# Performance work log

Measured on AMD Instinct MI355X. Metric: run time of the kernel, lower is better.

## Reference

```python
import jax, jax.numpy as jnp
import numpy as np

N_NODES = 20000   # max_childs
N_EDGES = 640000
FEAT = 256        # node_feat_size
HID = 128         # node_hidden_size
NUM_SEM = 57
EDGE_TYPES = 4
EDGE_FEAT = 8


def setup_inputs() -> dict:
    key = jax.random.key(0)
    ks = jax.random.split(key, 10)
    inp = {
        "child_feats": jax.random.normal(ks[0], (1, N_NODES, FEAT + NUM_SEM), jnp.float32),
        "child_exists": jnp.ones((1, N_NODES, 1), jnp.float32),
        "edge_type_onehot": jax.random.uniform(ks[1], (1, N_EDGES, EDGE_TYPES), jnp.float32),
        "edge_feats": jax.random.normal(ks[2], (1, N_EDGES, EDGE_FEAT), jnp.float32),
        "edge_indices": jax.random.randint(ks[3], (1, N_EDGES, 2), 0, N_NODES, jnp.int64 if jax.config.jax_enable_x64 else jnp.int32),
        "W_child": jax.random.normal(ks[4], (FEAT + NUM_SEM, HID), jnp.float32) * 0.05,
        "b_child": jnp.zeros((HID,), jnp.float32),
        "W_edge0": jax.random.normal(ks[5], (2 * HID + EDGE_FEAT + EDGE_TYPES, HID), jnp.float32) * 0.05,
        "b_edge0": jnp.zeros((HID,), jnp.float32),
        "W_edge1": jax.random.normal(ks[6], (2 * HID + EDGE_FEAT + EDGE_TYPES, HID), jnp.float32) * 0.05,
        "b_edge1": jnp.zeros((HID,), jnp.float32),
        "W_parent": jax.random.normal(ks[7], (3 * HID, FEAT), jnp.float32) * 0.05,
        "b_parent": jnp.zeros((FEAT,), jnp.float32),
    }
    return inp


def reference(child_feats, child_exists, edge_type_onehot, edge_feats, edge_indices,
              W_child, b_child, W_edge0, b_edge0, W_edge1, b_edge1, W_parent, b_parent):
    # child_op + existence mask: [1, N, FEAT+NUM_SEM] -> [N, HID]
    h = jax.nn.relu(child_feats @ W_child + b_child) * child_exists
    h = h[0]  # batch_size is hard-coded to 1 in the original module

    # symmetric_type == 'max': pool over children
    iter_parent_feats = [jnp.max(h, axis=0)]

    # edge features: cat(edge_type_onehot, edge_feats) -> [E, ET+EF]
    ef = jnp.concatenate([edge_type_onehot[0], edge_feats[0]], axis=1)
    src = edge_indices[0, :, 0]
    dst = edge_indices[0, :, 1]

    for W, b in ((W_edge0, b_edge0), (W_edge1, b_edge1)):
        # gather -> per-edge MLP: [E, 2*HID + ET + EF] -> [E, HID]
        msg = jax.nn.relu(jnp.concatenate([h[src], h[dst], ef], axis=1) @ W + b)
        # edge_symmetric_type == 'max' with zero-initialized out buffer:
        # result = max(0, segment_max(msg)) per node
        h = jnp.maximum(jax.ops.segment_max(msg, src, num_segments=N_NODES), 0.0)
        iter_parent_feats.append(jnp.max(h, axis=0))

    parent = jnp.concatenate(iter_parent_feats)[None, :]  # [1, 3*HID]
    return jax.nn.relu(parent @ W_parent + b_parent)       # [1, FEAT]
```

## Files before the change

kernel.cpp:

```cpp
#include <hip/hip_runtime.h>

#define N_NODES   20000
#define N_EDGES   640000
#define CF        313
#define KC        320
#define ROWB      640

typedef __attribute__((ext_vector_type(8))) short short8;
typedef __attribute__((ext_vector_type(4))) float f32x4;
typedef __attribute__((ext_vector_type(4))) unsigned short u16x4;
typedef float f32x4u __attribute__((ext_vector_type(4), aligned(4)));
typedef _Float16 h2 __attribute__((ext_vector_type(2)));

static __device__ __forceinline__ unsigned short f2bf(float f) {
    unsigned u = __float_as_uint(f);
    u = u + 0x7FFFu + ((u >> 16) & 1u);
    return (unsigned short)(u >> 16);
}
static __device__ __forceinline__ int pkh(float a, float b) {
    h2 h; h.x = (_Float16)a; h.y = (_Float16)b;
    return __builtin_bit_cast(int, h);
}
static __device__ __forceinline__ h2 bch(int v) { return __builtin_bit_cast(h2, v); }
static __device__ __forceinline__ float dot2f(h2 a, h2 b, float c) {
    return __builtin_amdgcn_fdot2(a, b, c, false);
}

__global__ void setup_kernel(const float* __restrict__ Wc,
                             const float* __restrict__ We0,
                             const float* __restrict__ We1,
                             const int* __restrict__ eidx,
                             unsigned short* __restrict__ WcT,
                             unsigned short* __restrict__ Wab0,
                             unsigned short* __restrict__ Wab1,
                             unsigned* __restrict__ hist) {
    const int b = blockIdx.x, tid = threadIdx.x;
    if (b < 416) {
        int g = b * 256 + tid;
        if (g < 128 * KC) {
            int n = g / KC, k = g % KC;
            WcT[g] = f2bf(k < CF ? Wc[k * 128 + n] : 0.f);
        } else if (g < 128 * KC + 32768) {
            int h = g - 128 * KC;
            int n = h >> 7, k = h & 127;
            Wab0[h] = f2bf(n < 128 ? We0[k * 128 + n] : We0[(128 + k) * 128 + (n - 128)]);
        } else {
            int h = g - 128 * KC - 32768;
            int n = h >> 7, k = h & 127;
            Wab1[h] = f2bf(n < 128 ? We1[k * 128 + n] : We1[(128 + k) * 128 + (n - 128)]);
        }
    } else {
        int e = (b - 416) * 256 + tid;
        if (e < N_EDGES) atomicAdd(hist + eidx[2 * e], 1u);
    }
}

__global__ void scan_kernel(const unsigned* __restrict__ hist,
                            unsigned* __restrict__ cursor,
                            unsigned* __restrict__ cstart,
                            unsigned* __restrict__ parent) {
    __shared__ unsigned part[1024];
    int t = threadIdx.x;
    if (t < 384) parent[t] = 0;
    unsigned loc[20];
    unsigned s = 0;
    int base = t * 20;
    if (t < 1000) {
        #pragma unroll
        for (int i = 0; i < 20; ++i) { loc[i] = hist[base + i]; s += loc[i]; }
    }
    part[t] = s;
    __syncthreads();
    for (int off = 1; off < 1024; off <<= 1) {
        unsigned u = (t >= off) ? part[t - off] : 0u;
        __syncthreads();
        part[t] += u;
        __syncthreads();
    }
    if (t < 1000) {
        unsigned run = part[t] - s;
        #pragma unroll
        for (int i = 0; i < 20; ++i) {
            cursor[base + i] = run;
            cstart[base + i] = run;
            run += loc[i];
        }
    }
}

__global__ void scatter_kernel(const int* __restrict__ eidx,
                               const float* __restrict__ onehot,
                               const float* __restrict__ efeat,
                               unsigned* __restrict__ cursor,
                               int4* __restrict__ es) {
    int e = blockIdx.x * 256 + threadIdx.x;
    if (e >= N_EDGES) return;
    int2 sd = ((const int2*)eidx)[e];
    unsigned pos = atomicAdd(cursor + sd.x, 1u);
    float4 oh = *(const float4*)(onehot + 4 * (size_t)e);
    float4 ea = *(const float4*)(efeat + 8 * (size_t)e);
    float4 eb = *(const float4*)(efeat + 8 * (size_t)e + 4);
    int4 w0, w1;
    w0.x = sd.y;
    w0.y = pkh(oh.x, oh.y); w0.z = pkh(oh.z, oh.w); w0.w = pkh(ea.x, ea.y);
    w1.x = pkh(ea.z, ea.w); w1.y = pkh(eb.x, eb.y); w1.z = pkh(eb.z, eb.w);
    w1.w = 0;
    es[2 * (size_t)pos]     = w0;
    es[2 * (size_t)pos + 1] = w1;
}

__global__ __launch_bounds__(256)
void child_ab(const float* __restrict__ cf,
              const float* __restrict__ exists,
              const unsigned short* __restrict__ WcT,
              const float* __restrict__ bc,
              const unsigned short* __restrict__ Wab,
              const float* __restrict__ be,
              float* __restrict__ Afl,
              unsigned short* __restrict__ Bbf,
              unsigned int* __restrict__ pmax) {
    __shared__ __align__(16) unsigned char Alds[64 * ROWB];
    __shared__ __align__(16) unsigned char Hlds[64 * 256];

    const int tid  = threadIdx.x;
    const int lane = tid & 63;
    const int wave = tid >> 6;
    const int row0 = blockIdx.x * 64;

    const int n0c = wave * 32;
    short8 bfrag[10][2];
    {
        int col  = n0c + (lane & 15);
        int krow = (lane >> 4) * 8;
        #pragma unroll
        for (int ks = 0; ks < 10; ++ks)
            #pragma unroll
            for (int nt = 0; nt < 2; ++nt)
                bfrag[ks][nt] = *(const short8*)(WcT + (col + nt * 16) * KC + ks * 32 + krow);
    }
    float bvc[2];
    bvc[0] = bc[n0c + (lane & 15)];
    bvc[1] = bc[n0c + 16 + (lane & 15)];

    {
        int r = tid >> 2, p = tid & 3;
        int node = row0 + r;
        bool valid = node < N_NODES;
        const float* g = cf + (size_t)node * CF;
        unsigned rbase = r * ROWB;
        unsigned sw = (r & 7) << 4;
        #pragma unroll
        for (int i = 0; i < 10; ++i) {
            int c = p + i * 4;
            short8 v = {};
            if (valid) {
                if (c < 39) {
                    f32x4u a0 = *(const f32x4u*)(g + c * 8);
                    f32x4u a1 = *(const f32x4u*)(g + c * 8 + 4);
                    v[0] = (short)f2bf(a0.x); v[1] = (short)f2bf(a0.y);
                    v[2] = (short)f2bf(a0.z); v[3] = (short)f2bf(a0.w);
                    v[4] = (short)f2bf(a1.x); v[5] = (short)f2bf(a1.y);
                    v[6] = (short)f2bf(a1.z); v[7] = (short)f2bf(a1.w);
                } else {
                    v[0] = (short)f2bf(g[312]);
                }
            }
            *(short8*)(Alds + ((rbase + c * 16) ^ sw)) = v;
        }
    }
    __syncthreads();

    f32x4 acc[4][2] = {};
    {
        int arow = lane & 15;
        unsigned kb = (lane >> 4) * 16;
        #pragma unroll
        for (int ks = 0; ks < 10; ++ks)
            #pragma unroll
            for (int mt = 0; mt < 4; ++mt) {
                int row = mt * 16 + arow;
                short8 a = *(const short8*)(Alds + (((unsigned)row * ROWB + ks * 64 + kb) ^ ((row & 7) << 4)));
                acc[mt][0] = __builtin_amdgcn_mfma_f32_16x16x32_bf16(a, bfrag[ks][0], acc[mt][0], 0, 0, 0);
                acc[mt][1] = __builtin_amdgcn_mfma_f32_16x16x32_bf16(a, bfrag[ks][1], acc[mt][1], 0, 0, 0);
            }
    }

    {
        int rb = (lane >> 4) * 4;
        #pragma unroll
        for (int nt = 0; nt < 2; ++nt) {
            int col = n0c + nt * 16 + (lane & 15);
            float m = 0.f;
            #pragma unroll
            for (int mt = 0; mt < 4; ++mt)
                #pragma unroll
                for (int j = 0; j < 4; ++j) {
                    int r = mt * 16 + rb + j;
                    int node = row0 + r;
                    float v = 0.f;
                    if (node < N_NODES)
                        v = fmaxf(acc[mt][nt][j] + bvc[nt], 0.f) * exists[node];
                    *(unsigned short*)(Hlds + (((unsigned)r * 256 + col * 2) ^ ((r & 7) << 4))) = f2bf(v);
                    m = fmaxf(m, v);
                }
            m = fmaxf(m, __shfl_xor(m, 16));
            m = fmaxf(m, __shfl_xor(m, 32));
            if ((lane >> 4) == 0)
                atomicMax(pmax + col, __float_as_uint(m));
        }
    }
    __syncthreads();

    const int n0 = wave * 64;
    const int krow = (lane >> 4) * 8;
    short8 bfrag2[4][4];
    {
        int colb = n0 + (lane & 15);
        #pragma unroll
        for (int ks = 0; ks < 4; ++ks)
            #pragma unroll
            for (int nt = 0; nt < 4; ++nt)
                bfrag2[ks][nt] = *(const short8*)(Wab + (colb + nt * 16) * 128 + ks * 32 + krow);
    }

    f32x4 acc2[4][4] = {};
    #pragma unroll
    for (int ks = 0; ks < 4; ++ks)
        #pragma unroll
        for (int mt = 0; mt < 4; ++mt) {
            int r = mt * 16 + (lane & 15);
            short8 a = *(const short8*)(Hlds + (((unsigned)r * 256 + ks * 64 + krow * 2) ^ ((r & 7) << 4)));
            #pragma unroll
            for (int nt = 0; nt < 4; ++nt)
                acc2[mt][nt] = __builtin_amdgcn_mfma_f32_16x16x32_bf16(a, bfrag2[ks][nt], acc2[mt][nt], 0, 0, 0);
        }

    {
        int rb = (lane >> 4) * 4;
        #pragma unroll
        for (int nt = 0; nt < 4; ++nt) {
            int col = n0 + nt * 16 + (lane & 15);
            float badd = (col < 128) ? be[col] : 0.f;
            #pragma unroll
            for (int mt = 0; mt < 4; ++mt)
                #pragma unroll
                for (int j = 0; j < 4; ++j) {
                    int row = row0 + mt * 16 + rb + j;
                    if (row < N_NODES) {
                        float v = acc2[mt][nt][j] + badd;
                        if (col < 128) Afl[(size_t)row * 128 + col] = v;
                        else           Bbf[(size_t)row * 128 + col - 128] = f2bf(v);
                    }
                }
        }
    }
}

__global__ __launch_bounds__(256)
void gemmAB(const unsigned short* __restrict__ hbf,
            const unsigned short* __restrict__ WT,
            const float* __restrict__ bias,
            float* __restrict__ Afl,
            unsigned short* __restrict__ Bbf) {
    const int tid  = threadIdx.x;
    const int lane = tid & 63;
    const int wave = tid >> 6;
    const int n0   = wave * 64;
    const int row0 = blockIdx.x * 32;
    const int krow = (lane >> 4) * 8;

    short8 bfrag[4][4];
    {
        int colb = n0 + (lane & 15);
        #pragma unroll
        for (int ks = 0; ks < 4; ++ks)
            #pragma unroll
            for (int nt = 0; nt < 4; ++nt)
                bfrag[ks][nt] = *(const short8*)(WT + (colb + nt * 16) * 128 + ks * 32 + krow);
    }

    f32x4 acc[2][4] = {};
    #pragma unroll
    for (int ks = 0; ks < 4; ++ks)
        #pragma unroll
        for (int mt = 0; mt < 2; ++mt) {
            int row = row0 + mt * 16 + (lane & 15);
            short8 a = *(const short8*)(hbf + (size_t)row * 128 + ks * 32 + krow);
            #pragma unroll
            for (int nt = 0; nt < 4; ++nt)
                acc[mt][nt] = __builtin_amdgcn_mfma_f32_16x16x32_bf16(a, bfrag[ks][nt], acc[mt][nt], 0, 0, 0);
        }

    {
        int rb = (lane >> 4) * 4;
        #pragma unroll
        for (int nt = 0; nt < 4; ++nt) {
            int col = n0 + nt * 16 + (lane & 15);
            float badd = (col < 128) ? bias[col] : 0.f;
            #pragma unroll
            for (int mt = 0; mt < 2; ++mt)
                #pragma unroll
                for (int j = 0; j < 4; ++j) {
                    int row = row0 + mt * 16 + rb + j;
                    float v = acc[mt][nt][j] + badd;
                    if (col < 128) Afl[(size_t)row * 128 + col] = v;
                    else           Bbf[(size_t)row * 128 + col - 128] = f2bf(v);
                }
        }
    }
}

__global__ __launch_bounds__(256, 3)
void edge_pass(const unsigned short* __restrict__ Bbf,
               const float* __restrict__ Afl,
               const int4* __restrict__ es,
               const float* __restrict__ Wef,
               const unsigned* __restrict__ cstart,
               const unsigned* __restrict__ hist,
               unsigned short* __restrict__ hbf,
               unsigned* __restrict__ pslice) {
    __shared__ unsigned cmax[128];
    const int tid = threadIdx.x;
    if (tid < 128) cmax[tid] = 0;
    __syncthreads();

    const int s  = blockIdx.x * 8 + (tid >> 5);
    const int c0 = (tid & 31) * 4;

    float4 a = *(const float4*)(Afl + (size_t)s * 128 + c0);

    h2 wf[6][4];
    #pragma unroll
    for (int kp = 0; kp < 6; ++kp)
        #pragma unroll
        for (int j = 0; j < 4; ++j) {
            h2 w;
            w.x = (_Float16)Wef[(2 * kp) * 128 + c0 + j];
            w.y = (_Float16)Wef[(2 * kp + 1) * 128 + c0 + j];
            wf[kp][j] = w;
        }

    float m0 = -1e30f, m1 = -1e30f, m2 = -1e30f, m3 = -1e30f;
    const unsigned cnt = hist[s];
    if (cnt) {
        const unsigned last = cnt - 1;
        const unsigned cb = cstart[s] * 32u;
        const char* esb = (const char*)es;
        const unsigned short* bbase = Bbf + c0;

        unsigned dstv[12];
        int4 ra[3], rb[3];
        u16x4 bv[6];

        #pragma unroll
        for (int k = 0; k < 12; ++k)
            dstv[k] = *(const unsigned*)(esb + cb + min((unsigned)k, last) * 32u);
        #pragma unroll
        for (int k = 0; k < 3; ++k) {
            const int4* q = (const int4*)(esb + cb + min((unsigned)k, last) * 32u);
            ra[k] = q[0]; rb[k] = q[1];
        }
        #pragma unroll
        for (int k = 0; k < 6; ++k)
            bv[k] = *(const u16x4*)(bbase + (size_t)dstv[k] * 128);

        const unsigned niter = (cnt + 11) / 12;
        for (unsigned it = 0; it < niter; ++it) {
            const unsigned jb = it * 12;
            #pragma unroll
            for (int u = 0; u < 12; ++u) {
                int4 RA = ra[u % 3], RB = rb[u % 3];
                u16x4 B = bv[u % 6];
                h2 e0 = bch(RA.y), e1 = bch(RA.z), e2 = bch(RA.w);
                h2 e3 = bch(RB.x), e4 = bch(RB.y), e5 = bch(RB.z);

                float x0 = __uint_as_float(((unsigned)(unsigned short)B[0]) << 16);
                float x1 = __uint_as_float(((unsigned)(unsigned short)B[1]) << 16);
                float x2 = __uint_as_float(((unsigned)(unsigned short)B[2]) << 16);
                float x3 = __uint_as_float(((unsigned)(unsigned short)B[3]) << 16);
                x0 = dot2f(e0, wf[0][0], x0); x1 = dot2f(e0, wf[0][1], x1);
                x2 = dot2f(e0, wf[0][2], x2); x3 = dot2f(e0, wf[0][3], x3);
                x0 = dot2f(e1, wf[1][0], x0); x1 = dot2f(e1, wf[1][1], x1);
                x2 = dot2f(e1, wf[1][2], x2); x3 = dot2f(e1, wf[1][3], x3);
                x0 = dot2f(e2, wf[2][0], x0); x1 = dot2f(e2, wf[2][1], x1);
                x2 = dot2f(e2, wf[2][2], x2); x3 = dot2f(e2, wf[2][3], x3);
                x0 = dot2f(e3, wf[3][0], x0); x1 = dot2f(e3, wf[3][1], x1);
                x2 = dot2f(e3, wf[3][2], x2); x3 = dot2f(e3, wf[3][3], x3);
                x0 = dot2f(e4, wf[4][0], x0); x1 = dot2f(e4, wf[4][1], x1);
                x2 = dot2f(e4, wf[4][2], x2); x3 = dot2f(e4, wf[4][3], x3);
                x0 = dot2f(e5, wf[5][0], x0); x1 = dot2f(e5, wf[5][1], x1);
                x2 = dot2f(e5, wf[5][2], x2); x3 = dot2f(e5, wf[5][3], x3);
                m0 = fmaxf(m0, x0); m1 = fmaxf(m1, x1);
                m2 = fmaxf(m2, x2); m3 = fmaxf(m3, x3);

                unsigned jd = min(jb + u + 12u, last);
                dstv[u] = *(const unsigned*)(esb + cb + jd * 32u);
                unsigned jr = min(jb + u + 3u, last);
                const int4* q = (const int4*)(esb + cb + jr * 32u);
                ra[u % 3] = q[0]; rb[u % 3] = q[1];
                bv[u % 6] = *(const u16x4*)(bbase + (size_t)dstv[(u + 6) % 12] * 128);
            }
        }
    }

    float h0 = fmaxf(a.x + m0, 0.f), h1 = fmaxf(a.y + m1, 0.f);
    float h2v = fmaxf(a.z + m2, 0.f), h3 = fmaxf(a.w + m3, 0.f);

    unsigned lo = (unsigned)f2bf(h0) | ((unsigned)f2bf(h1) << 16);
    unsigned hi = (unsigned)f2bf(h2v) | ((unsigned)f2bf(h3) << 16);
    *(uint2*)(hbf + (size_t)s * 128 + c0) = make_uint2(lo, hi);

    float g0 = fmaxf(h0, __shfl_xor(h0, 32));
    float g1 = fmaxf(h1, __shfl_xor(h1, 32));
    float g2 = fmaxf(h2v, __shfl_xor(h2v, 32));
    float g3 = fmaxf(h3, __shfl_xor(h3, 32));
    if ((tid & 63) < 32) {
        atomicMax(&cmax[c0],     __float_as_uint(g0));
        atomicMax(&cmax[c0 + 1], __float_as_uint(g1));
        atomicMax(&cmax[c0 + 2], __float_as_uint(g2));
        atomicMax(&cmax[c0 + 3], __float_as_uint(g3));
    }
    __syncthreads();
    if (tid < 128) atomicMax(pslice + tid, cmax[tid]);
}

__global__ void final_gemm(const float* __restrict__ parent,
                           const float* __restrict__ Wp,
                           const float* __restrict__ bp,
                           float* __restrict__ out) {
    __shared__ float p[384];
    __shared__ float red[256];
    int t = threadIdx.x;
    for (int i = t; i < 384; i += 256) p[i] = parent[i];
    __syncthreads();
    int col = blockIdx.x * 16 + (t & 15);
    int kc  = t >> 4;
    float s = 0.f;
    for (int k = kc * 24; k < kc * 24 + 24; ++k) s += p[k] * Wp[k * 256 + col];
    red[t] = s;
    __syncthreads();
    #pragma unroll
    for (int off = 8; off >= 1; off >>= 1) {
        if (kc < off) red[t] += red[t + off * 16];
        __syncthreads();
    }
    if (t < 16) out[col] = fmaxf(red[t] + bp[col], 0.f);
}

extern "C" void kernel_launch(void* const* d_in, const int* in_sizes, int n_in,
                              void* d_out, int out_size, void* d_ws, size_t ws_size,
                              hipStream_t stream) {
    const float* child_feats  = (const float*)d_in[0];
    const float* child_exists = (const float*)d_in[1];
    const float* onehot       = (const float*)d_in[2];
    const float* efeat        = (const float*)d_in[3];
    const int*   eidx         = (const int*)d_in[4];
    const float* Wc  = (const float*)d_in[5];
    const float* bc  = (const float*)d_in[6];
    const float* We0 = (const float*)d_in[7];
    const float* be0 = (const float*)d_in[8];
    const float* We1 = (const float*)d_in[9];
    const float* be1 = (const float*)d_in[10];
    const float* Wp  = (const float*)d_in[11];
    const float* bp  = (const float*)d_in[12];

    char* ws = (char*)d_ws;
    unsigned short* hbf    = (unsigned short*)(ws);
    float*          Afl    = (float*)(ws + 5120000);
    unsigned short* Bbf    = (unsigned short*)(ws + 15360000);
    int4*           es     = (int4*)(ws + 20480000);
    unsigned short* WcT    = (unsigned short*)(ws + 40960000);
    unsigned short* Wab0   = (unsigned short*)(ws + 41041920);
    unsigned short* Wab1   = (unsigned short*)(ws + 41107456);
    unsigned*       parent = (unsigned*)(ws + 41172992);
    unsigned*       hist   = (unsigned*)(ws + 41174528);
    unsigned*       cstart = (unsigned*)(ws + 41254528);
    unsigned*       cursor = (unsigned*)(ws + 41334592);

    const float* Wef0 = We0 + 256 * 128;
    const float* Wef1 = We1 + 256 * 128;

    hipMemsetAsync(hist, 0, N_NODES * 4, stream);

    setup_kernel<<<2916, 256, 0, stream>>>(Wc, We0, We1, eidx, WcT, Wab0, Wab1, hist);
    scan_kernel<<<1, 1024, 0, stream>>>(hist, cursor, cstart, parent);
    scatter_kernel<<<2500, 256, 0, stream>>>(eidx, onehot, efeat, cursor, es);

    child_ab<<<313, 256, 0, stream>>>(child_feats, child_exists, WcT, bc,
                                      Wab0, be0, Afl, Bbf, parent);

    edge_pass<<<2500, 256, 0, stream>>>(Bbf, Afl, es, Wef0, cstart, hist, hbf, parent + 128);

    gemmAB<<<625, 256, 0, stream>>>(hbf, Wab1, be1, Afl, Bbf);
    edge_pass<<<2500, 256, 0, stream>>>(Bbf, Afl, es, Wef1, cstart, hist, hbf, parent + 256);

    final_gemm<<<16, 256, 0, stream>>>((const float*)parent, Wp, bp, (float*)d_out);
}
```

Before: 264.3 us.

## Sort nodes by out-degree for edge_pass and halve child_ab tile rows

The scan kernel now builds a degree-sorted node order (a counting sort on in-block atomics, descending degree), and edge_pass maps each half-wave to a node through this order. Nodes in one block then have similar edge counts, which should cut warp and block imbalance in the per-node segment-max loops. Separately, child_ab processes 32 rows per block instead of 64, launching 625 blocks for better occupancy and CU coverage, and drops the bounds checks because 20000 is divisible by 32. The sort adds serial work in a single thread and scattered node indexing in edge_pass, so Afl and output accesses lose their locality.

Result: slower. 273.0 us (+3.3%).

```diff
diff --git a/kernel.cpp b/kernel.cpp
--- a/kernel.cpp
+++ b/kernel.cpp
@@ -58,10 +58,14 @@
 __global__ void scan_kernel(const unsigned* __restrict__ hist,
                             unsigned* __restrict__ cursor,
                             unsigned* __restrict__ cstart,
-                            unsigned* __restrict__ parent) {
+                            unsigned* __restrict__ parent,
+                            unsigned* __restrict__ sord) {
     __shared__ unsigned part[1024];
+    __shared__ unsigned dbin[256];
+    __shared__ unsigned doff[256];
     int t = threadIdx.x;
     if (t < 384) parent[t] = 0;
+    if (t < 256) dbin[t] = 0;
     unsigned loc[20];
     unsigned s = 0;
     int base = t * 20;
@@ -84,6 +88,23 @@
             cursor[base + i] = run;
             cstart[base + i] = run;
             run += loc[i];
+        }
+        #pragma unroll
+        for (int i = 0; i < 20; ++i)
+            atomicAdd(&dbin[min(loc[i], 255u)], 1u);
+    }
+    __syncthreads();
+    if (t == 0) {
+        unsigned run = 0;
+        for (int b = 255; b >= 0; --b) { doff[b] = run; run += dbin[b]; }
+    }
+    __syncthreads();
+    if (t < 1000) {
+        #pragma unroll
+        for (int i = 0; i < 20; ++i) {
+            unsigned b = min(loc[i], 255u);
+            unsigned p = atomicAdd(&doff[b], 1u);
+            sord[p] = (unsigned)(base + i);
         }
     }
 }
@@ -119,13 +140,13 @@
               float* __restrict__ Afl,
               unsigned short* __restrict__ Bbf,
               unsigned int* __restrict__ pmax) {
-    __shared__ __align__(16) unsigned char Alds[64 * ROWB];
-    __shared__ __align__(16) unsigned char Hlds[64 * 256];
+    __shared__ __align__(16) unsigned char Alds[32 * ROWB];
+    __shared__ __align__(16) unsigned char Hlds[32 * 256];
 
     const int tid  = threadIdx.x;
     const int lane = tid & 63;
     const int wave = tid >> 6;
-    const int row0 = blockIdx.x * 64;
+    const int row0 = blockIdx.x * 32;
 
     const int n0c = wave * 32;
     short8 bfrag[10][2];
@@ -143,41 +164,37 @@
     bvc[1] = bc[n0c + 16 + (lane & 15)];
 
     {
-        int r = tid >> 2, p = tid & 3;
-        int node = row0 + r;
-        bool valid = node < N_NODES;
-        const float* g = cf + (size_t)node * CF;
+        int r = tid >> 3, p = tid & 7;
+        const float* g = cf + (size_t)(row0 + r) * CF;
         unsigned rbase = r * ROWB;
         unsigned sw = (r & 7) << 4;
         #pragma unroll
-        for (int i = 0; i < 10; ++i) {
-            int c = p + i * 4;
+        for (int i = 0; i < 5; ++i) {
+            int c = p + i * 8;
             short8 v = {};
-            if (valid) {
-                if (c < 39) {
-                    f32x4u a0 = *(const f32x4u*)(g + c * 8);
-                    f32x4u a1 = *(const f32x4u*)(g + c * 8 + 4);
-                    v[0] = (short)f2bf(a0.x); v[1] = (short)f2bf(a0.y);
-                    v[2] = (short)f2bf(a0.z); v[3] = (short)f2bf(a0.w);
-                    v[4] = (short)f2bf(a1.x); v[5] = (short)f2bf(a1.y);
-                    v[6] = (short)f2bf(a1.z); v[7] = (short)f2bf(a1.w);
-                } else {
-                    v[0] = (short)f2bf(g[312]);
-                }
+            if (c < 39) {
+                f32x4u a0 = *(const f32x4u*)(g + c * 8);
+                f32x4u a1 = *(const f32x4u*)(g + c * 8 + 4);
+                v[0] = (short)f2bf(a0.x); v[1] = (short)f2bf(a0.y);
+                v[2] = (short)f2bf(a0.z); v[3] = (short)f2bf(a0.w);
+                v[4] = (short)f2bf(a1.x); v[5] = (short)f2bf(a1.y);
+                v[6] = (short)f2bf(a1.z); v[7] = (short)f2bf(a1.w);
+            } else {
+                v[0] = (short)f2bf(g[312]);
             }
             *(short8*)(Alds + ((rbase + c * 16) ^ sw)) = v;
         }
     }
     __syncthreads();
 
-    f32x4 acc[4][2] = {};
+    f32x4 acc[2][2] = {};
     {
         int arow = lane & 15;
         unsigned kb = (lane >> 4) * 16;
         #pragma unroll
         for (int ks = 0; ks < 10; ++ks)
             #pragma unroll
-            for (int mt = 0; mt < 4; ++mt) {
+            for (int mt = 0; mt < 2; ++mt) {
                 int row = mt * 16 + arow;
                 short8 a = *(const short8*)(Alds + (((unsigned)row * ROWB + ks * 64 + kb) ^ ((row & 7) << 4)));
                 acc[mt][0] = __builtin_amdgcn_mfma_f32_16x16x32_bf16(a, bfrag[ks][0], acc[mt][0], 0, 0, 0);
@@ -192,14 +209,11 @@
             int col = n0c + nt * 16 + (lane & 15);
             float m = 0.f;
             #pragma unroll
-            for (int mt = 0; mt < 4; ++mt)
+            for (int mt = 0; mt < 2; ++mt)
                 #pragma unroll
                 for (int j = 0; j < 4; ++j) {
                     int r = mt * 16 + rb + j;
-                    int node = row0 + r;
-                    float v = 0.f;
-                    if (node < N_NODES)
-                        v = fmaxf(acc[mt][nt][j] + bvc[nt], 0.f) * exists[node];
+                    float v = fmaxf(acc[mt][nt][j] + bvc[nt], 0.f) * exists[row0 + r];
                     *(unsigned short*)(Hlds + (((unsigned)r * 256 + col * 2) ^ ((r & 7) << 4))) = f2bf(v);
                     m = fmaxf(m, v);
                 }
@@ -223,11 +237,11 @@
                 bfrag2[ks][nt] = *(const short8*)(Wab + (colb + nt * 16) * 128 + ks * 32 + krow);
     }
 
-    f32x4 acc2[4][4] = {};
+    f32x4 acc2[2][4] = {};
     #pragma unroll
     for (int ks = 0; ks < 4; ++ks)
         #pragma unroll
-        for (int mt = 0; mt < 4; ++mt) {
+        for (int mt = 0; mt < 2; ++mt) {
             int r = mt * 16 + (lane & 15);
             short8 a = *(const short8*)(Hlds + (((unsigned)r * 256 + ks * 64 + krow * 2) ^ ((r & 7) << 4)));
             #pragma unroll
@@ -242,15 +256,13 @@
             int col = n0 + nt * 16 + (lane & 15);
             float badd = (col < 128) ? be[col] : 0.f;
             #pragma unroll
-            for (int mt = 0; mt < 4; ++mt)
+            for (int mt = 0; mt < 2; ++mt)
                 #pragma unroll
                 for (int j = 0; j < 4; ++j) {
                     int row = row0 + mt * 16 + rb + j;
-                    if (row < N_NODES) {
-                        float v = acc2[mt][nt][j] + badd;
-                        if (col < 128) Afl[(size_t)row * 128 + col] = v;
-                        else           Bbf[(size_t)row * 128 + col - 128] = f2bf(v);
-                    }
+                    float v = acc2[mt][nt][j] + badd;
+                    if (col < 128) Afl[(size_t)row * 128 + col] = v;
+                    else           Bbf[(size_t)row * 128 + col - 128] = f2bf(v);
                 }
         }
     }
@@ -317,6 +329,7 @@
                const float* __restrict__ Wef,
                const unsigned* __restrict__ cstart,
                const unsigned* __restrict__ hist,
+               const unsigned* __restrict__ sord,
                unsigned short* __restrict__ hbf,
                unsigned* __restrict__ pslice) {
     __shared__ unsigned cmax[128];
@@ -324,7 +337,7 @@
     if (tid < 128) cmax[tid] = 0;
     __syncthreads();
 
-    const int s  = blockIdx.x * 8 + (tid >> 5);
+    const int s  = (int)sord[blockIdx.x * 8 + (tid >> 5)];
     const int c0 = (tid & 31) * 4;
 
     float4 a = *(const float4*)(Afl + (size_t)s * 128 + c0);
@@ -476,6 +489,7 @@
     unsigned*       hist   = (unsigned*)(ws + 41174528);
     unsigned*       cstart = (unsigned*)(ws + 41254528);
     unsigned*       cursor = (unsigned*)(ws + 41334592);
+    unsigned*       sord   = (unsigned*)(ws + 41414592);
 
     const float* Wef0 = We0 + 256 * 128;
     const float* Wef1 = We1 + 256 * 128;
@@ -483,16 +497,18 @@
     hipMemsetAsync(hist, 0, N_NODES * 4, stream);
 
     setup_kernel<<<2916, 256, 0, stream>>>(Wc, We0, We1, eidx, WcT, Wab0, Wab1, hist);
-    scan_kernel<<<1, 1024, 0, stream>>>(hist, cursor, cstart, parent);
+    scan_kernel<<<1, 1024, 0, stream>>>(hist, cursor, cstart, parent, sord);
     scatter_kernel<<<2500, 256, 0, stream>>>(eidx, onehot, efeat, cursor, es);
 
-    child_ab<<<313, 256, 0, stream>>>(child_feats, child_exists, WcT, bc,
+    child_ab<<<625, 256, 0, stream>>>(child_feats, child_exists, WcT, bc,
                                       Wab0, be0, Afl, Bbf, parent);
 
-    edge_pass<<<2500, 256, 0, stream>>>(Bbf, Afl, es, Wef0, cstart, hist, hbf, parent + 128);
+    edge_pass<<<2500, 256, 0, stream>>>(Bbf, Afl, es, Wef0, cstart, hist, sord,
+                                        hbf, parent + 128);
 
     gemmAB<<<625, 256, 0, stream>>>(hbf, Wab1, be1, Afl, Bbf);
-    edge_pass<<<2500, 256, 0, stream>>>(Bbf, Afl, es, Wef1, cstart, hist, hbf, parent + 256);
+    edge_pass<<<2500, 256, 0, stream>>>(Bbf, Afl, es, Wef1, cstart, hist, sord,
+                                        hbf, parent + 256);
 
     final_gemm<<<16, 256, 0, stream>>>((const float*)parent, Wp, bp, (float*)d_out);
 }
```
